# Kernel tuning notes

Hardware: AMD Instinct MI355X
Metric: run time of the kernel (lower is better)

The kernel has to match this reference:

```python
import jax, jax.numpy as jnp
import numpy as np

N_NODES = 50000
N_EDGES = 1600000
IN_FEATS = 256
OUT_FEATS = 64


def setup_inputs() -> dict:
    key = jax.random.key(0)
    k1, k2, k3, k4, k5, k6 = jax.random.split(key, 6)
    feature = jax.random.normal(k1, (N_NODES, IN_FEATS), dtype=jnp.float32)
    src = jax.random.randint(k2, (N_EDGES,), 0, N_NODES, dtype=jnp.int32)
    dst = jax.random.randint(k3, (N_EDGES,), 0, N_NODES, dtype=jnp.int32)
    # parameters (xavier-ish scaling)
    W = jax.random.normal(k4, (OUT_FEATS, IN_FEATS), dtype=jnp.float32) * np.sqrt(2.0 / (IN_FEATS + OUT_FEATS))
    att_w = jax.random.normal(k5, (1, 2 * OUT_FEATS), dtype=jnp.float32) * np.sqrt(2.0 / (2 * OUT_FEATS + 1))
    bias = jax.random.normal(k6, (1, OUT_FEATS), dtype=jnp.float32) * np.sqrt(2.0 / (1 + OUT_FEATS))
    return {"feature": feature, "W": W, "att_w": att_w, "bias": bias, "src": src, "dst": dst}


def reference(feature, W, att_w, bias, src, dst):
    # Wh = linear(feature)   [N, out]
    Wh = feature @ W.T
    # concat([Wh_src, Wh_dst]) @ att_w.T  ==  Wh_src@a_src + Wh_dst@a_dst
    a_src = att_w[0, :OUT_FEATS]
    a_dst = att_w[0, OUT_FEATS:]
    el = Wh @ a_src  # [N]
    er = Wh @ a_dst  # [N]
    e = el[src] + er[dst]  # [E]
    e = jax.nn.leaky_relu(e, negative_slope=0.2)
    # segment softmax over incoming edges of each dst node
    e_max = jax.ops.segment_max(e, dst, num_segments=N_NODES)  # -inf for empty
    e_max = jnp.where(jnp.isfinite(e_max), e_max, 0.0)
    e_exp = jnp.exp(e - e_max[dst])
    denom = jax.ops.segment_sum(e_exp, dst, num_segments=N_NODES)
    alpha = e_exp / jnp.where(denom[dst] > 0, denom[dst], 1.0)  # [E]
    # scatter-weighted sum of source features
    h_new = jax.ops.segment_sum(alpha[:, None] * Wh[src], dst, num_segments=N_NODES)
    # residual + bias + activation
    h_new = h_new + Wh
    h_new = jax.nn.elu(h_new + bias)
    return h_new
```

## Files before the change

### kernel.cpp

```cpp
#include <hip/hip_runtime.h>
#include <hip/hip_bf16.h>
#include <math.h>

#define N_NODES 50000
#define N_EDGES 1600000
#define IN_F 256
#define OUT_F 64

#define NBUCKETS 196
#define CAP 10752
#define GEMM_BLOCKS 782
#define BK_BLOCKS 391
#define EPB 4096

typedef short short8 __attribute__((ext_vector_type(8)));
typedef unsigned short ushort8v __attribute__((ext_vector_type(8)));
typedef float f32x4 __attribute__((ext_vector_type(4)));

__device__ __forceinline__ unsigned short f2bf(float f) {
    union { __hip_bfloat16 h; unsigned short u; } v;
    v.h = __float2bfloat16(f);
    return v.u;
}
__device__ __forceinline__ float bf2f(unsigned u) {
    return __uint_as_float(u << 16);
}

__global__ __launch_bounds__(256) void k_prep(const float* __restrict__ W,
                                              unsigned short* __restrict__ wfrag,
                                              int* __restrict__ cnt) {
    const int tid = threadIdx.x;
    if (blockIdx.x == 0 && tid < NBUCKETS) cnt[tid] = 0;
    int c = blockIdx.x * 256 + tid;
    int ct = c >> 9, kt = (c >> 6) & 7, cl = c & 63;
    int col = ct * 16 + (cl & 15);
    int kb = kt * 32 + 8 * (cl >> 4);
    const float* p = W + col * 256 + kb;
    float4 x = *(const float4*)p;
    float4 y = *(const float4*)(p + 4);
    short8 v;
    v[0] = f2bf(x.x); v[1] = f2bf(x.y); v[2] = f2bf(x.z); v[3] = f2bf(x.w);
    v[4] = f2bf(y.x); v[5] = f2bf(y.y); v[6] = f2bf(y.z); v[7] = f2bf(y.w);
    *(short8*)(wfrag + c * 8) = v;
}

__global__ __launch_bounds__(256) void k_main(const float* __restrict__ feat,
                                              const unsigned short* __restrict__ wfrag,
                                              const float* __restrict__ att_w,
                                              unsigned short* __restrict__ whb,
                                              float* __restrict__ el,
                                              float* __restrict__ er,
                                              const int* __restrict__ src,
                                              const int* __restrict__ dst,
                                              int* __restrict__ cnt,
                                              unsigned* __restrict__ pairs) {
    __shared__ unsigned short wlds[16384];
    const int tid = threadIdx.x;

    if (blockIdx.x >= GEMM_BLOCKS) {
        int* lhist = (int*)wlds;
        int* lcur  = lhist + 256;
        const int bbeg = (blockIdx.x - GEMM_BLOCKS) * EPB;

        unsigned wreg[16];
        #pragma unroll
        for (int j = 0; j < 4; ++j) {
            int e0 = bbeg + j * 1024 + tid * 4;
            if (e0 + 3 < N_EDGES) {
                int4 dv = *(const int4*)(dst + e0);
                int4 sv = *(const int4*)(src + e0);
                wreg[j*4+0] = (unsigned)sv.x | ((unsigned)(dv.x & 255) << 16) | ((unsigned)(dv.x >> 8) << 24);
                wreg[j*4+1] = (unsigned)sv.y | ((unsigned)(dv.y & 255) << 16) | ((unsigned)(dv.y >> 8) << 24);
                wreg[j*4+2] = (unsigned)sv.z | ((unsigned)(dv.z & 255) << 16) | ((unsigned)(dv.z >> 8) << 24);
                wreg[j*4+3] = (unsigned)sv.w | ((unsigned)(dv.w & 255) << 16) | ((unsigned)(dv.w >> 8) << 24);
            } else {
                #pragma unroll
                for (int k = 0; k < 4; ++k) {
                    int e = e0 + k;
                    if (e < N_EDGES) {
                        int d = dst[e];
                        wreg[j*4+k] = (unsigned)src[e] | ((unsigned)(d & 255) << 16) | ((unsigned)(d >> 8) << 24);
                    } else wreg[j*4+k] = 0xFF000000u;
                }
            }
        }
        for (int i = tid; i < NBUCKETS; i += 256) lhist[i] = 0;
        __syncthreads();
        #pragma unroll
        for (int k = 0; k < 16; ++k) {
            unsigned b = wreg[k] >> 24;
            if (b < NBUCKETS) atomicAdd(&lhist[b], 1);
        }
        __syncthreads();
        for (int i = tid; i < NBUCKETS; i += 256) {
            int c = lhist[i];
            lcur[i] = c ? (i * CAP + atomicAdd(&cnt[i], c)) : 0;
        }
        __syncthreads();
        #pragma unroll
        for (int k = 0; k < 16; ++k) {
            unsigned wv = wreg[k];
            unsigned b = wv >> 24;
            if (b < NBUCKETS) {
                int pos = atomicAdd(&lcur[b], 1);
                pairs[pos] = wv & 0x00FFFFFFu;
            }
        }
        return;
    }

    const int l = tid & 63, w = tid >> 6;
    const int l15 = l & 15, lg = l >> 4;
    const int wbase = blockIdx.x * 64 + w * 16;
    int ar = wbase + l15; if (ar > N_NODES - 1) ar = N_NODES - 1;
    const float* fbase = feat + (size_t)ar * IN_F + 8 * lg;

    float4 f[16];
    #pragma unroll
    for (int kt = 0; kt < 8; ++kt) {
        f[2*kt]   = *(const float4*)(fbase + kt * 32);
        f[2*kt+1] = *(const float4*)(fbase + kt * 32 + 4);
    }
    #pragma unroll
    for (int i = 0; i < 8; ++i) {
        int c = tid + 256 * i;
        *(short8*)(&wlds[c * 8]) = *(const short8*)(wfrag + c * 8);
    }
    __builtin_amdgcn_sched_barrier(0);
    __syncthreads();

    f32x4 acc[4];
    #pragma unroll
    for (int ct = 0; ct < 4; ++ct) acc[ct] = (f32x4){0.f, 0.f, 0.f, 0.f};

    #pragma unroll
    for (int kt = 0; kt < 8; ++kt) {
        float4 fa = f[2*kt], fb = f[2*kt+1];
        short8 af;
        af[0] = f2bf(fa.x); af[1] = f2bf(fa.y); af[2] = f2bf(fa.z); af[3] = f2bf(fa.w);
        af[4] = f2bf(fb.x); af[5] = f2bf(fb.y); af[6] = f2bf(fb.z); af[7] = f2bf(fb.w);
        short8 b0 = *(const short8*)(&wlds[((0 * 8 + kt) * 64 + l) * 8]);
        short8 b1 = *(const short8*)(&wlds[((1 * 8 + kt) * 64 + l) * 8]);
        short8 b2 = *(const short8*)(&wlds[((2 * 8 + kt) * 64 + l) * 8]);
        short8 b3 = *(const short8*)(&wlds[((3 * 8 + kt) * 64 + l) * 8]);
        acc[0] = __builtin_amdgcn_mfma_f32_16x16x32_bf16(af, b0, acc[0], 0, 0, 0);
        acc[1] = __builtin_amdgcn_mfma_f32_16x16x32_bf16(af, b1, acc[1], 0, 0, 0);
        acc[2] = __builtin_amdgcn_mfma_f32_16x16x32_bf16(af, b2, acc[2], 0, 0, 0);
        acc[3] = __builtin_amdgcn_mfma_f32_16x16x32_bf16(af, b3, acc[3], 0, 0, 0);
    }

    float asrc[4], adst[4];
    #pragma unroll
    for (int ct = 0; ct < 4; ++ct) {
        asrc[ct] = att_w[ct * 16 + l15];
        adst[ct] = att_w[64 + ct * 16 + l15];
    }
    #pragma unroll
    for (int j = 0; j < 4; ++j) {
        int row = wbase + lg * 4 + j;
        float vs = 0.f, vd = 0.f;
        #pragma unroll
        for (int ct = 0; ct < 4; ++ct) {
            float v = acc[ct][j];
            vs += v * asrc[ct];
            vd += v * adst[ct];
            if (row < N_NODES) whb[(size_t)row * OUT_F + ct * 16 + l15] = f2bf(v);
        }
        vs += __shfl_xor(vs, 1); vd += __shfl_xor(vd, 1);
        vs += __shfl_xor(vs, 2); vd += __shfl_xor(vd, 2);
        vs += __shfl_xor(vs, 4); vd += __shfl_xor(vd, 4);
        vs += __shfl_xor(vs, 8); vd += __shfl_xor(vd, 8);
        if (l15 == 0 && row < N_NODES) { el[row] = vs; er[row] = vd; }
    }
}

__global__ __launch_bounds__(1024) void k_build(const int* __restrict__ cnt,
                                                const unsigned* __restrict__ pairs,
                                                const float* __restrict__ el,
                                                const float* __restrict__ er,
                                                int* __restrict__ offs,
                                                int* __restrict__ oend,
                                                unsigned* __restrict__ csr) {
    __shared__ int lcnt[256], ssc[256], lcur[256];
    __shared__ float ler[256];
    const int b = blockIdx.x;
    const int t = threadIdx.x;
    const int ebeg = b * CAP;
    const int nE = cnt[b];

    if (t < 256) {
        lcnt[t] = 0;
        int node = b * 256 + t;
        ler[t] = (node < N_NODES) ? er[node] : 0.f;
    }
    __syncthreads();
    for (int i = t; i < nE; i += 1024)
        atomicAdd(&lcnt[(pairs[ebeg + i] >> 16) & 255], 1);
    __syncthreads();
    if (t < 256) ssc[t] = (lcnt[t] + 7) & ~7;
    __syncthreads();
    for (int d = 1; d < 256; d <<= 1) {
        int v = 0;
        if (t < 256 && t >= d) v = ssc[t - d];
        __syncthreads();
        if (t < 256) ssc[t] += v;
        __syncthreads();
    }
    if (t < 256) {
        int pc = (lcnt[t] + 7) & ~7;
        int base = ssc[t] - pc;
        lcur[t] = base;
        int node = b * 256 + t;
        if (node < N_NODES) { offs[node] = ebeg + base; oend[node] = ebeg + base + pc; }
        for (int k = lcnt[t]; k < pc; ++k) csr[ebeg + base + k] = 0;
    }
    __syncthreads();
    for (int i = t; i < nE; i += 1024) {
        unsigned v = pairs[ebeg + i];
        int n8 = (v >> 16) & 255;
        int s = v & 0xFFFFu;
        float e = el[s] + ler[n8];
        e = (e > 0.f) ? e : 0.2f * e;
        float p = __expf(e);
        int pos = atomicAdd(&lcur[n8], 1);
        csr[ebeg + pos] = (unsigned)s | ((unsigned)f2bf(p) << 16);
    }
}

__global__ __launch_bounds__(256) void k_aggr(const int* __restrict__ offs,
                                              const int* __restrict__ oend,
                                              const unsigned* __restrict__ csr,
                                              const unsigned short* __restrict__ whb,
                                              const float* __restrict__ bias,
                                              float* __restrict__ out) {
    const int wid = __builtin_amdgcn_readfirstlane(threadIdx.x >> 6);
    const int node = blockIdx.x * 4 + wid;
    const int lane = threadIdx.x & 63;
    const int fg = lane & 7, es = lane >> 3;
    const int beg = offs[node], end = oend[node];

    float acc[8] = {0.f, 0.f, 0.f, 0.f, 0.f, 0.f, 0.f, 0.f};
    float den = 0.f;
    #pragma unroll 2
    for (int j = beg; j < end; j += 8) {
        unsigned e = csr[j + es];
        float p = __uint_as_float(e & 0xFFFF0000u);
        const unsigned short* wp = whb + (size_t)(e & 0xFFFFu) * OUT_F + fg * 8;
        ushort8v wv = *(const ushort8v*)wp;
        den += p;
        #pragma unroll
        for (int i = 0; i < 8; ++i) acc[i] = fmaf(p, bf2f((unsigned)wv[i]), acc[i]);
    }
    #pragma unroll
    for (int i = 0; i < 8; ++i) {
        acc[i] += __shfl_xor(acc[i], 8);
        acc[i] += __shfl_xor(acc[i], 16);
        acc[i] += __shfl_xor(acc[i], 32);
    }
    den += __shfl_xor(den, 8); den += __shfl_xor(den, 16); den += __shfl_xor(den, 32);

    if (es == 0) {
        float inv = (end > beg) ? 1.f / den : 0.f;
        ushort8v wn = *(const ushort8v*)(whb + (size_t)node * OUT_F + fg * 8);
        float4 b0 = *(const float4*)(bias + fg * 8);
        float4 b1 = *(const float4*)(bias + fg * 8 + 4);
        float h[8];
        h[0] = acc[0] * inv + bf2f((unsigned)wn[0]) + b0.x;
        h[1] = acc[1] * inv + bf2f((unsigned)wn[1]) + b0.y;
        h[2] = acc[2] * inv + bf2f((unsigned)wn[2]) + b0.z;
        h[3] = acc[3] * inv + bf2f((unsigned)wn[3]) + b0.w;
        h[4] = acc[4] * inv + bf2f((unsigned)wn[4]) + b1.x;
        h[5] = acc[5] * inv + bf2f((unsigned)wn[5]) + b1.y;
        h[6] = acc[6] * inv + bf2f((unsigned)wn[6]) + b1.z;
        h[7] = acc[7] * inv + bf2f((unsigned)wn[7]) + b1.w;
        #pragma unroll
        for (int i = 0; i < 8; ++i) h[i] = (h[i] > 0.f) ? h[i] : __expf(h[i]) - 1.f;
        float* op = out + (size_t)node * OUT_F + fg * 8;
        *(float4*)op = make_float4(h[0], h[1], h[2], h[3]);
        *(float4*)(op + 4) = make_float4(h[4], h[5], h[6], h[7]);
    }
}

extern "C" void kernel_launch(void* const* d_in, const int* in_sizes, int n_in,
                              void* d_out, int out_size, void* d_ws, size_t ws_size,
                              hipStream_t stream) {
    const float* feat  = (const float*)d_in[0];
    const float* W     = (const float*)d_in[1];
    const float* att_w = (const float*)d_in[2];
    const float* bias  = (const float*)d_in[3];
    const int*   src   = (const int*)d_in[4];
    const int*   dst   = (const int*)d_in[5];
    float* out = (float*)d_out;

    unsigned short* whb = (unsigned short*)d_ws;
    unsigned short* wfrag = whb + 3200000;
    float* el      = (float*)d_ws + 1600000 + 8192;
    float* er      = el + 50048;
    int*   offs    = (int*)(er + 50048);
    int*   oend    = offs + 50048;
    int*   cnt     = oend + 50048;
    unsigned* pairs = (unsigned*)(cnt + 512);
    unsigned* csr   = pairs + NBUCKETS * CAP;

    k_prep<<<8, 256, 0, stream>>>(W, wfrag, cnt);
    k_main<<<GEMM_BLOCKS + BK_BLOCKS, 256, 0, stream>>>(feat, wfrag, att_w, whb, el, er,
                                                        src, dst, cnt, pairs);
    k_build<<<NBUCKETS, 1024, 0, stream>>>(cnt, pairs, el, er, offs, oend, csr);
    k_aggr<<<N_NODES / 4, 256, 0, stream>>>(offs, oend, csr, whb, bias, out);
}
```

Baseline: 81.85 us.

## Fuse CSR build with aggregation and replace global bucket atomics with fixed runs

Drops the separate weight-prep kernel: each GEMM block converts W to bf16 fragments itself. Bucketing blocks now write fixed-size per-(bucket, block) runs of up to 64 edges plus a count, so no global atomic counters are needed. One 1024-thread kernel per bucket then gathers those runs, builds the per-node CSR in LDS, computes softmax weights and does the weighted gather with the ELU epilogue. This cuts four launches to two and avoids writing the CSR and offsets to global memory. The cost is redundant W conversion in every GEMM block, less parallelism in the aggregation phase, and edges silently dropped if any run exceeds 64 entries or a bucket's padded CSR overflows the LDS array.

```diff
diff --git a/kernel.cpp b/kernel.cpp
--- a/kernel.cpp
+++ b/kernel.cpp
@@ -7,11 +7,13 @@
 #define IN_F 256
 #define OUT_F 64
 
-#define NBUCKETS 196
-#define CAP 10752
+#define NB 196
+#define NBK 391
+#define EPB 4096
+#define RUN 64
 #define GEMM_BLOCKS 782
-#define BK_BLOCKS 391
-#define EPB 4096
+#define CSR_MAX 10752
+#define MAXRUNS 25
 
 typedef short short8 __attribute__((ext_vector_type(8)));
 typedef unsigned short ushort8v __attribute__((ext_vector_type(8)));
@@ -26,41 +28,23 @@
     return __uint_as_float(u << 16);
 }
 
-__global__ __launch_bounds__(256) void k_prep(const float* __restrict__ W,
-                                              unsigned short* __restrict__ wfrag,
-                                              int* __restrict__ cnt) {
-    const int tid = threadIdx.x;
-    if (blockIdx.x == 0 && tid < NBUCKETS) cnt[tid] = 0;
-    int c = blockIdx.x * 256 + tid;
-    int ct = c >> 9, kt = (c >> 6) & 7, cl = c & 63;
-    int col = ct * 16 + (cl & 15);
-    int kb = kt * 32 + 8 * (cl >> 4);
-    const float* p = W + col * 256 + kb;
-    float4 x = *(const float4*)p;
-    float4 y = *(const float4*)(p + 4);
-    short8 v;
-    v[0] = f2bf(x.x); v[1] = f2bf(x.y); v[2] = f2bf(x.z); v[3] = f2bf(x.w);
-    v[4] = f2bf(y.x); v[5] = f2bf(y.y); v[6] = f2bf(y.z); v[7] = f2bf(y.w);
-    *(short8*)(wfrag + c * 8) = v;
-}
-
 __global__ __launch_bounds__(256) void k_main(const float* __restrict__ feat,
-                                              const unsigned short* __restrict__ wfrag,
+                                              const float* __restrict__ W,
                                               const float* __restrict__ att_w,
                                               unsigned short* __restrict__ whb,
                                               float* __restrict__ el,
                                               float* __restrict__ er,
                                               const int* __restrict__ src,
                                               const int* __restrict__ dst,
-                                              int* __restrict__ cnt,
-                                              unsigned* __restrict__ pairs) {
+                                              unsigned* __restrict__ pairs,
+                                              int* __restrict__ runcnt) {
     __shared__ unsigned short wlds[16384];
     const int tid = threadIdx.x;
 
     if (blockIdx.x >= GEMM_BLOCKS) {
-        int* lhist = (int*)wlds;
-        int* lcur  = lhist + 256;
-        const int bbeg = (blockIdx.x - GEMM_BLOCKS) * EPB;
+        int* lcur = (int*)wlds;
+        const int bk = blockIdx.x - GEMM_BLOCKS;
+        const int bbeg = bk * EPB;
 
         unsigned wreg[16];
         #pragma unroll
@@ -84,27 +68,21 @@
                 }
             }
         }
-        for (int i = tid; i < NBUCKETS; i += 256) lhist[i] = 0;
-        __syncthreads();
-        #pragma unroll
-        for (int k = 0; k < 16; ++k) {
-            unsigned b = wreg[k] >> 24;
-            if (b < NBUCKETS) atomicAdd(&lhist[b], 1);
-        }
-        __syncthreads();
-        for (int i = tid; i < NBUCKETS; i += 256) {
-            int c = lhist[i];
-            lcur[i] = c ? (i * CAP + atomicAdd(&cnt[i], c)) : 0;
-        }
+        for (int i = tid; i < NB; i += 256) lcur[i] = 0;
         __syncthreads();
         #pragma unroll
         for (int k = 0; k < 16; ++k) {
             unsigned wv = wreg[k];
             unsigned b = wv >> 24;
-            if (b < NBUCKETS) {
+            if (b < NB) {
                 int pos = atomicAdd(&lcur[b], 1);
-                pairs[pos] = wv & 0x00FFFFFFu;
+                if (pos < RUN) pairs[((int)b * NBK + bk) * RUN + pos] = wv & 0x00FFFFFFu;
             }
+        }
+        __syncthreads();
+        for (int i = tid; i < NB; i += 256) {
+            int c = lcur[i];
+            runcnt[bk * NB + i] = (c < RUN) ? c : RUN;
         }
         return;
     }
@@ -124,7 +102,16 @@
     #pragma unroll
     for (int i = 0; i < 8; ++i) {
         int c = tid + 256 * i;
-        *(short8*)(&wlds[c * 8]) = *(const short8*)(wfrag + c * 8);
+        int ct = c >> 9, kt = (c >> 6) & 7, cl = c & 63;
+        int col = ct * 16 + (cl & 15);
+        int kb = kt * 32 + 8 * (cl >> 4);
+        const float* p = W + col * 256 + kb;
+        float4 x = *(const float4*)p;
+        float4 y = *(const float4*)(p + 4);
+        short8 v;
+        v[0] = f2bf(x.x); v[1] = f2bf(x.y); v[2] = f2bf(x.z); v[3] = f2bf(x.w);
+        v[4] = f2bf(y.x); v[5] = f2bf(y.y); v[6] = f2bf(y.z); v[7] = f2bf(y.w);
+        *(short8*)(&wlds[c * 8]) = v;
     }
     __builtin_amdgcn_sched_barrier(0);
     __syncthreads();
@@ -174,30 +161,44 @@
     }
 }
 
-__global__ __launch_bounds__(1024) void k_build(const int* __restrict__ cnt,
-                                                const unsigned* __restrict__ pairs,
-                                                const float* __restrict__ el,
-                                                const float* __restrict__ er,
-                                                int* __restrict__ offs,
-                                                int* __restrict__ oend,
-                                                unsigned* __restrict__ csr) {
-    __shared__ int lcnt[256], ssc[256], lcur[256];
+__global__ __launch_bounds__(1024) void k_fuse(const int* __restrict__ runcnt,
+                                               const unsigned* __restrict__ pairs,
+                                               const float* __restrict__ el,
+                                               const float* __restrict__ er,
+                                               const unsigned short* __restrict__ whb,
+                                               const float* __restrict__ bias,
+                                               float* __restrict__ out) {
+    __shared__ unsigned csr[CSR_MAX];
+    __shared__ int lcnt[256], ssc[256], lcur[256], obeg[256], olen[256];
     __shared__ float ler[256];
     const int b = blockIdx.x;
     const int t = threadIdx.x;
-    const int ebeg = b * CAP;
-    const int nE = cnt[b];
-
+    const int w = t >> 6, lane = t & 63;
+
+    for (int i = t; i < CSR_MAX; i += 1024) csr[i] = 0;
     if (t < 256) {
         lcnt[t] = 0;
         int node = b * 256 + t;
         ler[t] = (node < N_NODES) ? er[node] : 0.f;
     }
     __syncthreads();
-    for (int i = t; i < nE; i += 1024)
-        atomicAdd(&lcnt[(pairs[ebeg + i] >> 16) & 255], 1);
-    __syncthreads();
-    if (t < 256) ssc[t] = (lcnt[t] + 7) & ~7;
+
+    unsigned ent[MAXRUNS];
+    #pragma unroll
+    for (int it = 0; it < MAXRUNS; ++it) {
+        int r = w + it * 16;
+        unsigned e = 0xFFFFFFFFu;
+        if (r < NBK) {
+            int rc = runcnt[r * NB + b];
+            if (lane < rc) e = pairs[(b * NBK + r) * RUN + lane];
+        }
+        ent[it] = e;
+        if (e != 0xFFFFFFFFu) atomicAdd(&lcnt[(e >> 16) & 255], 1);
+    }
+    __syncthreads();
+
+    int pc = 0;
+    if (t < 256) { pc = (lcnt[t] + 7) & ~7; ssc[t] = pc; }
     __syncthreads();
     for (int d = 1; d < 256; d <<= 1) {
         int v = 0;
@@ -207,77 +208,74 @@
         __syncthreads();
     }
     if (t < 256) {
-        int pc = (lcnt[t] + 7) & ~7;
         int base = ssc[t] - pc;
         lcur[t] = base;
-        int node = b * 256 + t;
-        if (node < N_NODES) { offs[node] = ebeg + base; oend[node] = ebeg + base + pc; }
-        for (int k = lcnt[t]; k < pc; ++k) csr[ebeg + base + k] = 0;
-    }
-    __syncthreads();
-    for (int i = t; i < nE; i += 1024) {
-        unsigned v = pairs[ebeg + i];
-        int n8 = (v >> 16) & 255;
-        int s = v & 0xFFFFu;
-        float e = el[s] + ler[n8];
-        e = (e > 0.f) ? e : 0.2f * e;
-        float p = __expf(e);
-        int pos = atomicAdd(&lcur[n8], 1);
-        csr[ebeg + pos] = (unsigned)s | ((unsigned)f2bf(p) << 16);
-    }
-}
-
-__global__ __launch_bounds__(256) void k_aggr(const int* __restrict__ offs,
-                                              const int* __restrict__ oend,
-                                              const unsigned* __restrict__ csr,
-                                              const unsigned short* __restrict__ whb,
-                                              const float* __restrict__ bias,
-                                              float* __restrict__ out) {
-    const int wid = __builtin_amdgcn_readfirstlane(threadIdx.x >> 6);
-    const int node = blockIdx.x * 4 + wid;
-    const int lane = threadIdx.x & 63;
+        obeg[t] = base;
+        olen[t] = pc;
+    }
+    __syncthreads();
+
+    #pragma unroll
+    for (int it = 0; it < MAXRUNS; ++it) {
+        unsigned e = ent[it];
+        if (e != 0xFFFFFFFFu) {
+            int n8 = (e >> 16) & 255;
+            int s = e & 0xFFFFu;
+            float x = el[s] + ler[n8];
+            x = (x > 0.f) ? x : 0.2f * x;
+            float p = __expf(x);
+            int pos = atomicAdd(&lcur[n8], 1);
+            csr[pos] = (unsigned)s | ((unsigned)f2bf(p) << 16);
+        }
+    }
+    __syncthreads();
+
     const int fg = lane & 7, es = lane >> 3;
-    const int beg = offs[node], end = oend[node];
-
-    float acc[8] = {0.f, 0.f, 0.f, 0.f, 0.f, 0.f, 0.f, 0.f};
-    float den = 0.f;
-    #pragma unroll 2
-    for (int j = beg; j < end; j += 8) {
-        unsigned e = csr[j + es];
-        float p = __uint_as_float(e & 0xFFFF0000u);
-        const unsigned short* wp = whb + (size_t)(e & 0xFFFFu) * OUT_F + fg * 8;
-        ushort8v wv = *(const ushort8v*)wp;
-        den += p;
+    for (int j = 0; j < 16; ++j) {
+        int nl = w * 16 + j;
+        int node = b * 256 + nl;
+        if (node >= N_NODES) break;
+        int beg = obeg[nl], end = beg + olen[nl];
+        float acc[8] = {0.f, 0.f, 0.f, 0.f, 0.f, 0.f, 0.f, 0.f};
+        float den = 0.f;
+        #pragma unroll 2
+        for (int jj = beg; jj < end; jj += 8) {
+            unsigned e = csr[jj + es];
+            float p = __uint_as_float(e & 0xFFFF0000u);
+            const unsigned short* wp = whb + (size_t)(e & 0xFFFFu) * OUT_F + fg * 8;
+            ushort8v wv = *(const ushort8v*)wp;
+            den += p;
+            #pragma unroll
+            for (int i = 0; i < 8; ++i) acc[i] = fmaf(p, bf2f((unsigned)wv[i]), acc[i]);
+        }
         #pragma unroll
-        for (int i = 0; i < 8; ++i) acc[i] = fmaf(p, bf2f((unsigned)wv[i]), acc[i]);
-    }
-    #pragma unroll
-    for (int i = 0; i < 8; ++i) {
-        acc[i] += __shfl_xor(acc[i], 8);
-        acc[i] += __shfl_xor(acc[i], 16);
-        acc[i] += __shfl_xor(acc[i], 32);
-    }
-    den += __shfl_xor(den, 8); den += __shfl_xor(den, 16); den += __shfl_xor(den, 32);
-
-    if (es == 0) {
-        float inv = (end > beg) ? 1.f / den : 0.f;
-        ushort8v wn = *(const ushort8v*)(whb + (size_t)node * OUT_F + fg * 8);
-        float4 b0 = *(const float4*)(bias + fg * 8);
-        float4 b1 = *(const float4*)(bias + fg * 8 + 4);
-        float h[8];
-        h[0] = acc[0] * inv + bf2f((unsigned)wn[0]) + b0.x;
-        h[1] = acc[1] * inv + bf2f((unsigned)wn[1]) + b0.y;
-        h[2] = acc[2] * inv + bf2f((unsigned)wn[2]) + b0.z;
-        h[3] = acc[3] * inv + bf2f((unsigned)wn[3]) + b0.w;
-        h[4] = acc[4] * inv + bf2f((unsigned)wn[4]) + b1.x;
-        h[5] = acc[5] * inv + bf2f((unsigned)wn[5]) + b1.y;
-        h[6] = acc[6] * inv + bf2f((unsigned)wn[6]) + b1.z;
-        h[7] = acc[7] * inv + bf2f((unsigned)wn[7]) + b1.w;
-        #pragma unroll
-        for (int i = 0; i < 8; ++i) h[i] = (h[i] > 0.f) ? h[i] : __expf(h[i]) - 1.f;
-        float* op = out + (size_t)node * OUT_F + fg * 8;
-        *(float4*)op = make_float4(h[0], h[1], h[2], h[3]);
-        *(float4*)(op + 4) = make_float4(h[4], h[5], h[6], h[7]);
+        for (int i = 0; i < 8; ++i) {
+            acc[i] += __shfl_xor(acc[i], 8);
+            acc[i] += __shfl_xor(acc[i], 16);
+            acc[i] += __shfl_xor(acc[i], 32);
+        }
+        den += __shfl_xor(den, 8); den += __shfl_xor(den, 16); den += __shfl_xor(den, 32);
+
+        if (es == 0) {
+            float inv = (end > beg) ? 1.f / den : 0.f;
+            ushort8v wn = *(const ushort8v*)(whb + (size_t)node * OUT_F + fg * 8);
+            float4 b0 = *(const float4*)(bias + fg * 8);
+            float4 b1 = *(const float4*)(bias + fg * 8 + 4);
+            float h[8];
+            h[0] = acc[0] * inv + bf2f((unsigned)wn[0]) + b0.x;
+            h[1] = acc[1] * inv + bf2f((unsigned)wn[1]) + b0.y;
+            h[2] = acc[2] * inv + bf2f((unsigned)wn[2]) + b0.z;
+            h[3] = acc[3] * inv + bf2f((unsigned)wn[3]) + b0.w;
+            h[4] = acc[4] * inv + bf2f((unsigned)wn[4]) + b1.x;
+            h[5] = acc[5] * inv + bf2f((unsigned)wn[5]) + b1.y;
+            h[6] = acc[6] * inv + bf2f((unsigned)wn[6]) + b1.z;
+            h[7] = acc[7] * inv + bf2f((unsigned)wn[7]) + b1.w;
+            #pragma unroll
+            for (int i = 0; i < 8; ++i) h[i] = (h[i] > 0.f) ? h[i] : __expf(h[i]) - 1.f;
+            float* op = out + (size_t)node * OUT_F + fg * 8;
+            *(float4*)op = make_float4(h[0], h[1], h[2], h[3]);
+            *(float4*)(op + 4) = make_float4(h[4], h[5], h[6], h[7]);
+        }
     }
 }
 
@@ -293,18 +291,12 @@
     float* out = (float*)d_out;
 
     unsigned short* whb = (unsigned short*)d_ws;
-    unsigned short* wfrag = whb + 3200000;
-    float* el      = (float*)d_ws + 1600000 + 8192;
-    float* er      = el + 50048;
-    int*   offs    = (int*)(er + 50048);
-    int*   oend    = offs + 50048;
-    int*   cnt     = oend + 50048;
-    unsigned* pairs = (unsigned*)(cnt + 512);
-    unsigned* csr   = pairs + NBUCKETS * CAP;
-
-    k_prep<<<8, 256, 0, stream>>>(W, wfrag, cnt);
-    k_main<<<GEMM_BLOCKS + BK_BLOCKS, 256, 0, stream>>>(feat, wfrag, att_w, whb, el, er,
-                                                        src, dst, cnt, pairs);
-    k_build<<<NBUCKETS, 1024, 0, stream>>>(cnt, pairs, el, er, offs, oend, csr);
-    k_aggr<<<N_NODES / 4, 256, 0, stream>>>(offs, oend, csr, whb, bias, out);
-}
+    float* el       = (float*)d_ws + 1600000;
+    float* er       = el + 50048;
+    unsigned* pairs = (unsigned*)(er + 50048);
+    int* runcnt     = (int*)(pairs + NB * NBK * RUN);
+
+    k_main<<<GEMM_BLOCKS + NBK, 256, 0, stream>>>(feat, W, att_w, whb, el, er,
+                                                  src, dst, pairs, runcnt);
+    k_fuse<<<NB, 1024, 0, stream>>>(runcnt, pairs, el, er, whb, bias, out);
+}
```

After: 88.50 us. 1.08x slower.

## Fold weight prep into GEMM, double bucket count, pad CSR to 16

Applied to the files above, without the earlier changes.

Removes the separate weight-conversion kernel: each GEMM block now converts W from fp32 to bf16 fragments itself, and the bucket counter is zeroed with a memset. Buckets shrink from 256 to 128 destination nodes, so 391 build blocks run instead of 196. Per-node CSR segments are padded to multiples of 16, and the aggregation loop handles two 8-edge groups per iteration for more memory-level parallelism. The trade-offs are more padding edges to read and redundant W conversion in every GEMM block.

```diff
diff --git a/kernel.cpp b/kernel.cpp
--- a/kernel.cpp
+++ b/kernel.cpp
@@ -7,11 +7,11 @@
 #define IN_F 256
 #define OUT_F 64
 
-#define NBUCKETS 196
-#define CAP 10752
-#define GEMM_BLOCKS 782
+#define NB 391
+#define CAP 6400
 #define BK_BLOCKS 391
 #define EPB 4096
+#define GEMM_BLOCKS 782
 
 typedef short short8 __attribute__((ext_vector_type(8)));
 typedef unsigned short ushort8v __attribute__((ext_vector_type(8)));
@@ -26,26 +26,8 @@
     return __uint_as_float(u << 16);
 }
 
-__global__ __launch_bounds__(256) void k_prep(const float* __restrict__ W,
-                                              unsigned short* __restrict__ wfrag,
-                                              int* __restrict__ cnt) {
-    const int tid = threadIdx.x;
-    if (blockIdx.x == 0 && tid < NBUCKETS) cnt[tid] = 0;
-    int c = blockIdx.x * 256 + tid;
-    int ct = c >> 9, kt = (c >> 6) & 7, cl = c & 63;
-    int col = ct * 16 + (cl & 15);
-    int kb = kt * 32 + 8 * (cl >> 4);
-    const float* p = W + col * 256 + kb;
-    float4 x = *(const float4*)p;
-    float4 y = *(const float4*)(p + 4);
-    short8 v;
-    v[0] = f2bf(x.x); v[1] = f2bf(x.y); v[2] = f2bf(x.z); v[3] = f2bf(x.w);
-    v[4] = f2bf(y.x); v[5] = f2bf(y.y); v[6] = f2bf(y.z); v[7] = f2bf(y.w);
-    *(short8*)(wfrag + c * 8) = v;
-}
-
 __global__ __launch_bounds__(256) void k_main(const float* __restrict__ feat,
-                                              const unsigned short* __restrict__ wfrag,
+                                              const float* __restrict__ W,
                                               const float* __restrict__ att_w,
                                               unsigned short* __restrict__ whb,
                                               float* __restrict__ el,
@@ -59,7 +41,7 @@
 
     if (blockIdx.x >= GEMM_BLOCKS) {
         int* lhist = (int*)wlds;
-        int* lcur  = lhist + 256;
+        int* lcur  = lhist + 512;
         const int bbeg = (blockIdx.x - GEMM_BLOCKS) * EPB;
 
         unsigned wreg[16];
@@ -69,30 +51,30 @@
             if (e0 + 3 < N_EDGES) {
                 int4 dv = *(const int4*)(dst + e0);
                 int4 sv = *(const int4*)(src + e0);
-                wreg[j*4+0] = (unsigned)sv.x | ((unsigned)(dv.x & 255) << 16) | ((unsigned)(dv.x >> 8) << 24);
-                wreg[j*4+1] = (unsigned)sv.y | ((unsigned)(dv.y & 255) << 16) | ((unsigned)(dv.y >> 8) << 24);
-                wreg[j*4+2] = (unsigned)sv.z | ((unsigned)(dv.z & 255) << 16) | ((unsigned)(dv.z >> 8) << 24);
-                wreg[j*4+3] = (unsigned)sv.w | ((unsigned)(dv.w & 255) << 16) | ((unsigned)(dv.w >> 8) << 24);
+                wreg[j*4+0] = (unsigned)sv.x | ((unsigned)(dv.x & 127) << 16) | ((unsigned)(dv.x >> 7) << 23);
+                wreg[j*4+1] = (unsigned)sv.y | ((unsigned)(dv.y & 127) << 16) | ((unsigned)(dv.y >> 7) << 23);
+                wreg[j*4+2] = (unsigned)sv.z | ((unsigned)(dv.z & 127) << 16) | ((unsigned)(dv.z >> 7) << 23);
+                wreg[j*4+3] = (unsigned)sv.w | ((unsigned)(dv.w & 127) << 16) | ((unsigned)(dv.w >> 7) << 23);
             } else {
                 #pragma unroll
                 for (int k = 0; k < 4; ++k) {
                     int e = e0 + k;
                     if (e < N_EDGES) {
                         int d = dst[e];
-                        wreg[j*4+k] = (unsigned)src[e] | ((unsigned)(d & 255) << 16) | ((unsigned)(d >> 8) << 24);
-                    } else wreg[j*4+k] = 0xFF000000u;
+                        wreg[j*4+k] = (unsigned)src[e] | ((unsigned)(d & 127) << 16) | ((unsigned)(d >> 7) << 23);
+                    } else wreg[j*4+k] = 511u << 23;
                 }
             }
         }
-        for (int i = tid; i < NBUCKETS; i += 256) lhist[i] = 0;
+        for (int i = tid; i < NB; i += 256) lhist[i] = 0;
         __syncthreads();
         #pragma unroll
         for (int k = 0; k < 16; ++k) {
-            unsigned b = wreg[k] >> 24;
-            if (b < NBUCKETS) atomicAdd(&lhist[b], 1);
-        }
-        __syncthreads();
-        for (int i = tid; i < NBUCKETS; i += 256) {
+            unsigned b = wreg[k] >> 23;
+            if (b < NB) atomicAdd(&lhist[b], 1);
+        }
+        __syncthreads();
+        for (int i = tid; i < NB; i += 256) {
             int c = lhist[i];
             lcur[i] = c ? (i * CAP + atomicAdd(&cnt[i], c)) : 0;
         }
@@ -100,10 +82,10 @@
         #pragma unroll
         for (int k = 0; k < 16; ++k) {
             unsigned wv = wreg[k];
-            unsigned b = wv >> 24;
-            if (b < NBUCKETS) {
+            unsigned b = wv >> 23;
+            if (b < NB) {
                 int pos = atomicAdd(&lcur[b], 1);
-                pairs[pos] = wv & 0x00FFFFFFu;
+                pairs[pos] = wv & 0x007FFFFFu;
             }
         }
         return;
@@ -124,7 +106,16 @@
     #pragma unroll
     for (int i = 0; i < 8; ++i) {
         int c = tid + 256 * i;
-        *(short8*)(&wlds[c * 8]) = *(const short8*)(wfrag + c * 8);
+        int ct = c >> 9, kt = (c >> 6) & 7, cl = c & 63;
+        int col = ct * 16 + (cl & 15);
+        int kb = kt * 32 + 8 * (cl >> 4);
+        const float* p = W + col * 256 + kb;
+        float4 x = *(const float4*)p;
+        float4 y = *(const float4*)(p + 4);
+        short8 v;
+        v[0] = f2bf(x.x); v[1] = f2bf(x.y); v[2] = f2bf(x.z); v[3] = f2bf(x.w);
+        v[4] = f2bf(y.x); v[5] = f2bf(y.y); v[6] = f2bf(y.z); v[7] = f2bf(y.w);
+        *(short8*)(&wlds[c * 8]) = v;
     }
     __builtin_amdgcn_sched_barrier(0);
     __syncthreads();
@@ -181,48 +172,48 @@
                                                 int* __restrict__ offs,
                                                 int* __restrict__ oend,
                                                 unsigned* __restrict__ csr) {
-    __shared__ int lcnt[256], ssc[256], lcur[256];
-    __shared__ float ler[256];
+    __shared__ int lcnt[128], ssc[128], lcur[128];
+    __shared__ float ler[128];
     const int b = blockIdx.x;
     const int t = threadIdx.x;
     const int ebeg = b * CAP;
     const int nE = cnt[b];
 
-    if (t < 256) {
+    if (t < 128) {
         lcnt[t] = 0;
-        int node = b * 256 + t;
+        int node = b * 128 + t;
         ler[t] = (node < N_NODES) ? er[node] : 0.f;
     }
     __syncthreads();
     for (int i = t; i < nE; i += 1024)
-        atomicAdd(&lcnt[(pairs[ebeg + i] >> 16) & 255], 1);
-    __syncthreads();
-    if (t < 256) ssc[t] = (lcnt[t] + 7) & ~7;
-    __syncthreads();
-    for (int d = 1; d < 256; d <<= 1) {
+        atomicAdd(&lcnt[(pairs[ebeg + i] >> 16) & 127], 1);
+    __syncthreads();
+    if (t < 128) ssc[t] = (lcnt[t] + 15) & ~15;
+    __syncthreads();
+    for (int d = 1; d < 128; d <<= 1) {
         int v = 0;
-        if (t < 256 && t >= d) v = ssc[t - d];
-        __syncthreads();
-        if (t < 256) ssc[t] += v;
-        __syncthreads();
-    }
-    if (t < 256) {
-        int pc = (lcnt[t] + 7) & ~7;
+        if (t < 128 && t >= d) v = ssc[t - d];
+        __syncthreads();
+        if (t < 128) ssc[t] += v;
+        __syncthreads();
+    }
+    if (t < 128) {
+        int pc = (lcnt[t] + 15) & ~15;
         int base = ssc[t] - pc;
         lcur[t] = base;
-        int node = b * 256 + t;
+        int node = b * 128 + t;
         if (node < N_NODES) { offs[node] = ebeg + base; oend[node] = ebeg + base + pc; }
         for (int k = lcnt[t]; k < pc; ++k) csr[ebeg + base + k] = 0;
     }
     __syncthreads();
     for (int i = t; i < nE; i += 1024) {
         unsigned v = pairs[ebeg + i];
-        int n8 = (v >> 16) & 255;
+        int n7 = (v >> 16) & 127;
         int s = v & 0xFFFFu;
-        float e = el[s] + ler[n8];
+        float e = el[s] + ler[n7];
         e = (e > 0.f) ? e : 0.2f * e;
         float p = __expf(e);
-        int pos = atomicAdd(&lcur[n8], 1);
+        int pos = atomicAdd(&lcur[n7], 1);
         csr[ebeg + pos] = (unsigned)s | ((unsigned)f2bf(p) << 16);
     }
 }
@@ -241,15 +232,18 @@
 
     float acc[8] = {0.f, 0.f, 0.f, 0.f, 0.f, 0.f, 0.f, 0.f};
     float den = 0.f;
-    #pragma unroll 2
-    for (int j = beg; j < end; j += 8) {
-        unsigned e = csr[j + es];
-        float p = __uint_as_float(e & 0xFFFF0000u);
-        const unsigned short* wp = whb + (size_t)(e & 0xFFFFu) * OUT_F + fg * 8;
-        ushort8v wv = *(const ushort8v*)wp;
-        den += p;
-        #pragma unroll
-        for (int i = 0; i < 8; ++i) acc[i] = fmaf(p, bf2f((unsigned)wv[i]), acc[i]);
+    for (int jj = beg; jj < end; jj += 16) {
+        unsigned e0 = csr[jj + es];
+        unsigned e1 = csr[jj + 8 + es];
+        float p0 = __uint_as_float(e0 & 0xFFFF0000u);
+        float p1 = __uint_as_float(e1 & 0xFFFF0000u);
+        ushort8v wv0 = *(const ushort8v*)(whb + (size_t)(e0 & 0xFFFFu) * OUT_F + fg * 8);
+        ushort8v wv1 = *(const ushort8v*)(whb + (size_t)(e1 & 0xFFFFu) * OUT_F + fg * 8);
+        den += p0 + p1;
+        #pragma unroll
+        for (int i = 0; i < 8; ++i) acc[i] = fmaf(p0, bf2f((unsigned)wv0[i]), acc[i]);
+        #pragma unroll
+        for (int i = 0; i < 8; ++i) acc[i] = fmaf(p1, bf2f((unsigned)wv1[i]), acc[i]);
     }
     #pragma unroll
     for (int i = 0; i < 8; ++i) {
@@ -293,18 +287,17 @@
     float* out = (float*)d_out;
 
     unsigned short* whb = (unsigned short*)d_ws;
-    unsigned short* wfrag = whb + 3200000;
-    float* el      = (float*)d_ws + 1600000 + 8192;
-    float* er      = el + 50048;
-    int*   offs    = (int*)(er + 50048);
-    int*   oend    = offs + 50048;
-    int*   cnt     = oend + 50048;
+    float* el       = (float*)d_ws + 1600000;
+    float* er       = el + 50048;
+    int*   offs     = (int*)(er + 50048);
+    int*   oend     = offs + 50048;
+    int*   cnt      = oend + 50048;
     unsigned* pairs = (unsigned*)(cnt + 512);
-    unsigned* csr   = pairs + NBUCKETS * CAP;
-
-    k_prep<<<8, 256, 0, stream>>>(W, wfrag, cnt);
-    k_main<<<GEMM_BLOCKS + BK_BLOCKS, 256, 0, stream>>>(feat, wfrag, att_w, whb, el, er,
+    unsigned* csr   = pairs + NB * CAP;
+
+    hipMemsetAsync(cnt, 0, NB * sizeof(int), stream);
+    k_main<<<GEMM_BLOCKS + BK_BLOCKS, 256, 0, stream>>>(feat, W, att_w, whb, el, er,
                                                         src, dst, cnt, pairs);
-    k_build<<<NBUCKETS, 1024, 0, stream>>>(cnt, pairs, el, er, offs, oend, csr);
+    k_build<<<NB, 1024, 0, stream>>>(cnt, pairs, el, er, offs, oend, csr);
     k_aggr<<<N_NODES / 4, 256, 0, stream>>>(offs, oend, csr, whb, bias, out);
 }
```

Result: slower. 87.08 us (+6.4%).

## Quantize Wh to int8 with per-row scale and precompute softmax denominators

Applied to the files above, without the earlier changes.

Stores the projected features as int8 with a per-row scale instead of bf16, halving the bytes gathered per edge in the aggregation kernel. The per-row scale is folded into the bf16 edge weight when the CSR is built. Softmax denominators are now summed once in the build kernel via shared-memory atomics rather than reduced inside aggregation. The output layout is permuted so each lane's packed bytes map to interleaved columns. The cost is extra quantization error from int8 storage, plus LDS float atomics in the build kernel.

```diff
diff --git a/kernel.cpp b/kernel.cpp
--- a/kernel.cpp
+++ b/kernel.cpp
@@ -7,14 +7,13 @@
 #define IN_F 256
 #define OUT_F 64
 
-#define NBUCKETS 196
+#define NB 196
 #define CAP 10752
-#define GEMM_BLOCKS 782
 #define BK_BLOCKS 391
 #define EPB 4096
+#define GEMM_BLOCKS 782
 
 typedef short short8 __attribute__((ext_vector_type(8)));
-typedef unsigned short ushort8v __attribute__((ext_vector_type(8)));
 typedef float f32x4 __attribute__((ext_vector_type(4)));
 
 __device__ __forceinline__ unsigned short f2bf(float f) {
@@ -30,7 +29,7 @@
                                               unsigned short* __restrict__ wfrag,
                                               int* __restrict__ cnt) {
     const int tid = threadIdx.x;
-    if (blockIdx.x == 0 && tid < NBUCKETS) cnt[tid] = 0;
+    if (blockIdx.x == 0 && tid < NB) cnt[tid] = 0;
     int c = blockIdx.x * 256 + tid;
     int ct = c >> 9, kt = (c >> 6) & 7, cl = c & 63;
     int col = ct * 16 + (cl & 15);
@@ -47,7 +46,8 @@
 __global__ __launch_bounds__(256) void k_main(const float* __restrict__ feat,
                                               const unsigned short* __restrict__ wfrag,
                                               const float* __restrict__ att_w,
-                                              unsigned short* __restrict__ whb,
+                                              unsigned* __restrict__ whq32,
+                                              float* __restrict__ wscale,
                                               float* __restrict__ el,
                                               float* __restrict__ er,
                                               const int* __restrict__ src,
@@ -84,24 +84,24 @@
                 }
             }
         }
-        for (int i = tid; i < NBUCKETS; i += 256) lhist[i] = 0;
+        if (tid < NB) lhist[tid] = 0;
         __syncthreads();
         #pragma unroll
         for (int k = 0; k < 16; ++k) {
             unsigned b = wreg[k] >> 24;
-            if (b < NBUCKETS) atomicAdd(&lhist[b], 1);
-        }
-        __syncthreads();
-        for (int i = tid; i < NBUCKETS; i += 256) {
-            int c = lhist[i];
-            lcur[i] = c ? (i * CAP + atomicAdd(&cnt[i], c)) : 0;
+            if (b < NB) atomicAdd(&lhist[b], 1);
+        }
+        __syncthreads();
+        if (tid < NB) {
+            int c = lhist[tid];
+            lcur[tid] = c ? (tid * CAP + atomicAdd(&cnt[tid], c)) : 0;
         }
         __syncthreads();
         #pragma unroll
         for (int k = 0; k < 16; ++k) {
             unsigned wv = wreg[k];
             unsigned b = wv >> 24;
-            if (b < NBUCKETS) {
+            if (b < NB) {
                 int pos = atomicAdd(&lcur[b], 1);
                 pairs[pos] = wv & 0x00FFFFFFu;
             }
@@ -158,19 +158,25 @@
     #pragma unroll
     for (int j = 0; j < 4; ++j) {
         int row = wbase + lg * 4 + j;
-        float vs = 0.f, vd = 0.f;
-        #pragma unroll
-        for (int ct = 0; ct < 4; ++ct) {
-            float v = acc[ct][j];
-            vs += v * asrc[ct];
-            vd += v * adst[ct];
-            if (row < N_NODES) whb[(size_t)row * OUT_F + ct * 16 + l15] = f2bf(v);
-        }
-        vs += __shfl_xor(vs, 1); vd += __shfl_xor(vd, 1);
-        vs += __shfl_xor(vs, 2); vd += __shfl_xor(vd, 2);
-        vs += __shfl_xor(vs, 4); vd += __shfl_xor(vd, 4);
-        vs += __shfl_xor(vs, 8); vd += __shfl_xor(vd, 8);
-        if (l15 == 0 && row < N_NODES) { el[row] = vs; er[row] = vd; }
+        float v0 = acc[0][j], v1 = acc[1][j], v2 = acc[2][j], v3 = acc[3][j];
+        float vs = v0 * asrc[0] + v1 * asrc[1] + v2 * asrc[2] + v3 * asrc[3];
+        float vd = v0 * adst[0] + v1 * adst[1] + v2 * adst[2] + v3 * adst[3];
+        float mx = fmaxf(fmaxf(fabsf(v0), fabsf(v1)), fmaxf(fabsf(v2), fabsf(v3)));
+        vs += __shfl_xor(vs, 1); vd += __shfl_xor(vd, 1); mx = fmaxf(mx, __shfl_xor(mx, 1));
+        vs += __shfl_xor(vs, 2); vd += __shfl_xor(vd, 2); mx = fmaxf(mx, __shfl_xor(mx, 2));
+        vs += __shfl_xor(vs, 4); vd += __shfl_xor(vd, 4); mx = fmaxf(mx, __shfl_xor(mx, 4));
+        vs += __shfl_xor(vs, 8); vd += __shfl_xor(vd, 8); mx = fmaxf(mx, __shfl_xor(mx, 8));
+        float inv_s = (mx > 0.f) ? 127.f / mx : 0.f;
+        int q0 = __float2int_rn(v0 * inv_s);
+        int q1 = __float2int_rn(v1 * inv_s);
+        int q2 = __float2int_rn(v2 * inv_s);
+        int q3 = __float2int_rn(v3 * inv_s);
+        unsigned qp = (unsigned)(q0 & 255) | ((unsigned)(q1 & 255) << 8) |
+                      ((unsigned)(q2 & 255) << 16) | ((unsigned)(q3 & 255) << 24);
+        if (row < N_NODES) {
+            whq32[row * 16 + l15] = qp;
+            if (l15 == 0) { el[row] = vs; er[row] = vd; wscale[row] = mx * (1.f / 127.f); }
+        }
     }
 }
 
@@ -178,18 +184,20 @@
                                                 const unsigned* __restrict__ pairs,
                                                 const float* __restrict__ el,
                                                 const float* __restrict__ er,
+                                                const float* __restrict__ wscale,
                                                 int* __restrict__ offs,
                                                 int* __restrict__ oend,
+                                                float* __restrict__ denom,
                                                 unsigned* __restrict__ csr) {
     __shared__ int lcnt[256], ssc[256], lcur[256];
-    __shared__ float ler[256];
+    __shared__ float ler[256], lden[256];
     const int b = blockIdx.x;
     const int t = threadIdx.x;
     const int ebeg = b * CAP;
     const int nE = cnt[b];
 
     if (t < 256) {
-        lcnt[t] = 0;
+        lcnt[t] = 0; lden[t] = 0.f;
         int node = b * 256 + t;
         ler[t] = (node < N_NODES) ? er[node] : 0.f;
     }
@@ -223,14 +231,22 @@
         e = (e > 0.f) ? e : 0.2f * e;
         float p = __expf(e);
         int pos = atomicAdd(&lcur[n8], 1);
-        csr[ebeg + pos] = (unsigned)s | ((unsigned)f2bf(p) << 16);
+        csr[ebeg + pos] = (unsigned)s | ((unsigned)f2bf(p * wscale[s]) << 16);
+        atomicAdd(&lden[n8], p);
+    }
+    __syncthreads();
+    if (t < 256) {
+        int node = b * 256 + t;
+        if (node < N_NODES) denom[node] = lden[t];
     }
 }
 
 __global__ __launch_bounds__(256) void k_aggr(const int* __restrict__ offs,
                                               const int* __restrict__ oend,
                                               const unsigned* __restrict__ csr,
-                                              const unsigned short* __restrict__ whb,
+                                              const float* __restrict__ denom,
+                                              const unsigned char* __restrict__ whq,
+                                              const float* __restrict__ wscale,
                                               const float* __restrict__ bias,
                                               float* __restrict__ out) {
     const int wid = __builtin_amdgcn_readfirstlane(threadIdx.x >> 6);
@@ -240,16 +256,17 @@
     const int beg = offs[node], end = oend[node];
 
     float acc[8] = {0.f, 0.f, 0.f, 0.f, 0.f, 0.f, 0.f, 0.f};
-    float den = 0.f;
     #pragma unroll 2
-    for (int j = beg; j < end; j += 8) {
-        unsigned e = csr[j + es];
+    for (int jj = beg; jj < end; jj += 8) {
+        unsigned e = csr[jj + es];
         float p = __uint_as_float(e & 0xFFFF0000u);
-        const unsigned short* wp = whb + (size_t)(e & 0xFFFFu) * OUT_F + fg * 8;
-        ushort8v wv = *(const ushort8v*)wp;
-        den += p;
-        #pragma unroll
-        for (int i = 0; i < 8; ++i) acc[i] = fmaf(p, bf2f((unsigned)wv[i]), acc[i]);
+        uint2 wq = *(const uint2*)(whq + (size_t)(e & 0xFFFFu) * 64 + fg * 8);
+        #pragma unroll
+        for (int i = 0; i < 4; ++i)
+            acc[i] = fmaf(p, (float)(int)(signed char)((wq.x >> (8 * i)) & 255u), acc[i]);
+        #pragma unroll
+        for (int i = 0; i < 4; ++i)
+            acc[4 + i] = fmaf(p, (float)(int)(signed char)((wq.y >> (8 * i)) & 255u), acc[4 + i]);
     }
     #pragma unroll
     for (int i = 0; i < 8; ++i) {
@@ -257,27 +274,26 @@
         acc[i] += __shfl_xor(acc[i], 16);
         acc[i] += __shfl_xor(acc[i], 32);
     }
-    den += __shfl_xor(den, 8); den += __shfl_xor(den, 16); den += __shfl_xor(den, 32);
 
     if (es == 0) {
-        float inv = (end > beg) ? 1.f / den : 0.f;
-        ushort8v wn = *(const ushort8v*)(whb + (size_t)node * OUT_F + fg * 8);
-        float4 b0 = *(const float4*)(bias + fg * 8);
-        float4 b1 = *(const float4*)(bias + fg * 8 + 4);
+        float inv = (end > beg) ? 1.f / denom[node] : 0.f;
+        uint2 wqn = *(const uint2*)(whq + (size_t)node * 64 + fg * 8);
+        float sc_n = wscale[node];
         float h[8];
-        h[0] = acc[0] * inv + bf2f((unsigned)wn[0]) + b0.x;
-        h[1] = acc[1] * inv + bf2f((unsigned)wn[1]) + b0.y;
-        h[2] = acc[2] * inv + bf2f((unsigned)wn[2]) + b0.z;
-        h[3] = acc[3] * inv + bf2f((unsigned)wn[3]) + b0.w;
-        h[4] = acc[4] * inv + bf2f((unsigned)wn[4]) + b1.x;
-        h[5] = acc[5] * inv + bf2f((unsigned)wn[5]) + b1.y;
-        h[6] = acc[6] * inv + bf2f((unsigned)wn[6]) + b1.z;
-        h[7] = acc[7] * inv + bf2f((unsigned)wn[7]) + b1.w;
-        #pragma unroll
-        for (int i = 0; i < 8; ++i) h[i] = (h[i] > 0.f) ? h[i] : __expf(h[i]) - 1.f;
-        float* op = out + (size_t)node * OUT_F + fg * 8;
-        *(float4*)op = make_float4(h[0], h[1], h[2], h[3]);
-        *(float4*)(op + 4) = make_float4(h[4], h[5], h[6], h[7]);
+        #pragma unroll
+        for (int i = 0; i < 4; ++i) {
+            h[i]     = acc[i]     * inv + sc_n * (float)(int)(signed char)((wqn.x >> (8 * i)) & 255u);
+            h[4 + i] = acc[4 + i] * inv + sc_n * (float)(int)(signed char)((wqn.y >> (8 * i)) & 255u);
+        }
+        #pragma unroll
+        for (int ct = 0; ct < 4; ++ct) {
+            float2 bb = *(const float2*)(bias + ct * 16 + 2 * fg);
+            float x0 = h[ct] + bb.x;
+            float x1 = h[ct + 4] + bb.y;
+            x0 = (x0 > 0.f) ? x0 : __expf(x0) - 1.f;
+            x1 = (x1 > 0.f) ? x1 : __expf(x1) - 1.f;
+            *(float2*)(out + (size_t)node * OUT_F + ct * 16 + 2 * fg) = make_float2(x0, x1);
+        }
     }
 }
 
@@ -292,19 +308,22 @@
     const int*   dst   = (const int*)d_in[5];
     float* out = (float*)d_out;
 
-    unsigned short* whb = (unsigned short*)d_ws;
-    unsigned short* wfrag = whb + 3200000;
-    float* el      = (float*)d_ws + 1600000 + 8192;
+    unsigned* whq32 = (unsigned*)d_ws;
+    unsigned short* wfrag = (unsigned short*)(whq32 + 800000);
+    float* el      = (float*)(whq32 + 800000 + 8192);
     float* er      = el + 50048;
-    int*   offs    = (int*)(er + 50048);
+    float* wscale  = er + 50048;
+    float* denom   = wscale + 50048;
+    int*   offs    = (int*)(denom + 50048);
     int*   oend    = offs + 50048;
     int*   cnt     = oend + 50048;
     unsigned* pairs = (unsigned*)(cnt + 512);
-    unsigned* csr   = pairs + NBUCKETS * CAP;
+    unsigned* csr   = pairs + NB * CAP;
 
     k_prep<<<8, 256, 0, stream>>>(W, wfrag, cnt);
-    k_main<<<GEMM_BLOCKS + BK_BLOCKS, 256, 0, stream>>>(feat, wfrag, att_w, whb, el, er,
-                                                        src, dst, cnt, pairs);
-    k_build<<<NBUCKETS, 1024, 0, stream>>>(cnt, pairs, el, er, offs, oend, csr);
-    k_aggr<<<N_NODES / 4, 256, 0, stream>>>(offs, oend, csr, whb, bias, out);
-}
+    k_main<<<GEMM_BLOCKS + BK_BLOCKS, 256, 0, stream>>>(feat, wfrag, att_w, whq32, wscale,
+                                                        el, er, src, dst, cnt, pairs);
+    k_build<<<NB, 1024, 0, stream>>>(cnt, pairs, el, er, wscale, offs, oend, denom, csr);
+    k_aggr<<<N_NODES / 4, 256, 0, stream>>>(offs, oend, csr, denom,
+                                            (const unsigned char*)whq32, wscale, bias, out);
+}
```

Result: slower. 87.52 us (+6.9%).
